# Kernel tuning notes

Hardware: AMD Instinct MI355X
Metric: run time of the kernel (lower is better)

## Reference

```python
import jax, jax.numpy as jnp
import numpy as np

V, S, B, D, H, DH, FF = 98304, 1536, 2, 768, 24, 32, 3072
SCALE = 1.0 / float(np.sqrt(DH))  # 0.17677669529663687


def _ln(x, w, b, eps=1e-5):
    mu = jnp.mean(x, axis=-1, keepdims=True)
    var = jnp.mean(jnp.square(x - mu), axis=-1, keepdims=True)
    return (x - mu) * jax.lax.rsqrt(var + eps) * w + b


def _block(x, mask, ln1w, ln1b, wqkv, bqkv, wo, bo, ln2w, ln2b, wfc, bfc, wproj, bproj):
    # x: (S, B, D) Megatron layout; mask: (B, 1, S, S) bool, True = masked
    h = _ln(x, ln1w, ln1b)
    qkv = (h @ wqkv.T + bqkv).reshape(S, B, H, 3 * DH)  # interleaved q/k/v per head
    q, k, v = qkv[..., :DH], qkv[..., DH:2 * DH], qkv[..., 2 * DH:]
    q = jnp.transpose(q, (1, 2, 0, 3))  # (B, H, S, DH)
    k = jnp.transpose(k, (1, 2, 0, 3))
    v = jnp.transpose(v, (1, 2, 0, 3))
    scores = jnp.einsum('bhqd,bhkd->bhqk', q, k) * SCALE  # (B, H, S, S)
    scores = jnp.where(mask, jnp.float32(-10000.0), scores)
    p = jax.nn.softmax(scores, axis=-1)
    ctx = jnp.einsum('bhqk,bhkd->bhqd', p, v)
    ctx = jnp.transpose(ctx, (2, 0, 1, 3)).reshape(S, B, D)  # back to (S, B, D)
    x = x + ctx @ wo.T + bo  # attention residual (dropout treated as identity)
    h2 = _ln(x, ln2w, ln2b)
    m = jax.nn.gelu(h2 @ wfc.T + bfc, approximate=False)  # exact (erf) gelu as aten.gelu
    return x + m @ wproj.T + bproj


def _param_shapes():
    ps = [('wte', (V, D)), ('wpe', (S, D))]
    for l in ('l0', 'l1'):
        ps += [(l + '_ln1_w', (D,)), (l + '_ln1_b', (D,)),
               (l + '_wqkv', (3 * D, D)), (l + '_bqkv', (3 * D,)),
               (l + '_wo', (D, D)), (l + '_bo', (D,)),
               (l + '_ln2_w', (D,)), (l + '_ln2_b', (D,)),
               (l + '_wfc', (FF, D)), (l + '_bfc', (FF,)),
               (l + '_wproj', (D, FF)), (l + '_bproj', (D,))]
    ps += [('lnf_w', (D,)), ('lnf_b', (D,))]
    return ps


def setup_inputs() -> dict:
    key = jax.random.key(0)
    inp = {}
    inp['input_ids'] = jax.random.randint(jax.random.fold_in(key, 0), (B, S), 0, V, dtype=jnp.int32)
    inp['position_ids'] = jnp.broadcast_to(jnp.arange(S, dtype=jnp.int32), (B, S))
    causal = jnp.triu(jnp.ones((S, S), jnp.bool_), k=1)  # True above diagonal = masked
    inp['attn_mask'] = jnp.broadcast_to(causal, (B, 1, S, S))
    for i, (name, shape) in enumerate(_param_shapes()):
        k = jax.random.fold_in(key, 100 + i)
        if name in ('lnf_w',) or (('_ln' in name) and name.endswith('_w')):
            inp[name] = jnp.ones(shape, jnp.float32)
        else:
            inp[name] = jax.random.normal(k, shape, jnp.float32) * 0.02
    return inp


def reference(input_ids, position_ids, attn_mask,
              wte, wpe,
              l0_ln1_w, l0_ln1_b, l0_wqkv, l0_bqkv, l0_wo, l0_bo,
              l0_ln2_w, l0_ln2_b, l0_wfc, l0_bfc, l0_wproj, l0_bproj,
              l1_ln1_w, l1_ln1_b, l1_wqkv, l1_bqkv, l1_wo, l1_bo,
              l1_ln2_w, l1_ln2_b, l1_wfc, l1_bfc, l1_wproj, l1_bproj,
              lnf_w, lnf_b):
    x = wte[input_ids] + wpe[position_ids]  # (B, S, D)
    x = jnp.transpose(x, (1, 0, 2))  # (S, B, D)
    x = _block(x, attn_mask, l0_ln1_w, l0_ln1_b, l0_wqkv, l0_bqkv, l0_wo, l0_bo,
               l0_ln2_w, l0_ln2_b, l0_wfc, l0_bfc, l0_wproj, l0_bproj)
    x = _block(x, attn_mask, l1_ln1_w, l1_ln1_b, l1_wqkv, l1_bqkv, l1_wo, l1_bo,
               l1_ln2_w, l1_ln2_b, l1_wfc, l1_bfc, l1_wproj, l1_bproj)
    return _ln(x, lnf_w, lnf_b)  # (S, B, D)
```

## Files before the change

kernel.cpp:

```cpp
#include <hip/hip_runtime.h>
#include <cmath>
#include <type_traits>

typedef unsigned short u16;
typedef float  f32x4 __attribute__((ext_vector_type(4)));
typedef short  s16x8 __attribute__((ext_vector_type(8)));
typedef __bf16 b16x8 __attribute__((ext_vector_type(8)));

constexpr int S_  = 1536;
constexpr int B_  = 2;
constexpr int D_  = 768;
constexpr int H_  = 24;
constexpr int DH_ = 32;
constexpr int FF_ = 3072;
constexpr int N_  = S_ * B_;
constexpr int D3_ = 3 * D_;
constexpr float SCALE_ = 0.17677669529663687f;

template <typename T>
static __device__ inline auto mfma_try(T a, T b, f32x4 c, int)
    -> decltype(__builtin_amdgcn_mfma_f32_16x16x32_bf16(a, b, c, 0, 0, 0)) {
  return __builtin_amdgcn_mfma_f32_16x16x32_bf16(a, b, c, 0, 0, 0);
}
template <typename T>
static __device__ inline f32x4 mfma_try(T a, T b, f32x4 c, long) {
  b16x8 ab = __builtin_bit_cast(b16x8, a);
  b16x8 bb = __builtin_bit_cast(b16x8, b);
  return __builtin_amdgcn_mfma_f32_16x16x32_bf16(ab, bb, c, 0, 0, 0);
}
static __device__ inline f32x4 mfma_bf16(s16x8 a, s16x8 b, f32x4 c) {
  return mfma_try(a, b, c, 0);
}

static __device__ inline u16 f2bf(float f) {
  unsigned u = __builtin_bit_cast(unsigned, f);
  return (u16)((u + 0x7FFFu + ((u >> 16) & 1u)) >> 16);
}

static __device__ inline float rmax16(float v) {
  v = fmaxf(v, __shfl_xor(v, 1));
  v = fmaxf(v, __shfl_xor(v, 2));
  v = fmaxf(v, __shfl_xor(v, 4));
  v = fmaxf(v, __shfl_xor(v, 8));
  return v;
}
static __device__ inline float rsum16(float v) {
  v += __shfl_xor(v, 1);
  v += __shfl_xor(v, 2);
  v += __shfl_xor(v, 4);
  v += __shfl_xor(v, 8);
  return v;
}

__global__ void convert_weights_kernel(const float* __restrict__ wqkv,
                                       const float* __restrict__ wo,
                                       const float* __restrict__ wfc,
                                       const float* __restrict__ wproj,
                                       u16* __restrict__ dst) {
  constexpr int C0 = D3_ * D_;
  constexpr int C1 = C0 + D_ * D_;
  constexpr int C2 = C1 + FF_ * D_;
  constexpr int C3 = C2 + D_ * FF_;
  int i4 = (blockIdx.x * 256 + threadIdx.x) * 4;
  if (i4 >= C3) return;
  const float* src; int off;
  if (i4 < C0)      { src = wqkv;  off = i4; }
  else if (i4 < C1) { src = wo;    off = i4 - C0; }
  else if (i4 < C2) { src = wfc;   off = i4 - C1; }
  else              { src = wproj; off = i4 - C2; }
  float4 v = *(const float4*)(src + off);
  ushort4 o;
  o.x = f2bf(v.x); o.y = f2bf(v.y); o.z = f2bf(v.z); o.w = f2bf(v.w);
  *(ushort4*)(dst + i4) = o;
}

__global__ void embed_kernel(const int* __restrict__ ids, const int* __restrict__ pos,
                             const float* __restrict__ wte, const float* __restrict__ wpe,
                             float* __restrict__ x) {
  int g  = blockIdx.x * 256 + threadIdx.x;
  int i4 = g * 4;
  int row = i4 / D_;
  int d   = i4 - row * D_;
  int s = row >> 1, b = row & 1;
  int t = ids[b * S_ + s];
  int p = pos[b * S_ + s];
  float4 a = *(const float4*)(wte + (size_t)t * D_ + d);
  float4 c = *(const float4*)(wpe + (size_t)p * D_ + d);
  a.x += c.x; a.y += c.y; a.z += c.z; a.w += c.w;
  *(float4*)(x + i4) = a;
}

template <typename OUT>
__global__ void ln_kernel(const float* __restrict__ x, const float* __restrict__ w,
                          const float* __restrict__ b, OUT* __restrict__ out) {
  int wid = threadIdx.x >> 6, lane = threadIdx.x & 63;
  int tok = blockIdx.x * 4 + wid;
  const float* xr = x + (size_t)tok * D_;
  float4 v[3];
  float s = 0.f, ss = 0.f;
#pragma unroll
  for (int c = 0; c < 3; ++c) {
    v[c] = *(const float4*)(xr + c * 256 + lane * 4);
    s  += v[c].x + v[c].y + v[c].z + v[c].w;
    ss += v[c].x * v[c].x + v[c].y * v[c].y + v[c].z * v[c].z + v[c].w * v[c].w;
  }
#pragma unroll
  for (int m = 1; m <= 32; m <<= 1) { s += __shfl_xor(s, m); ss += __shfl_xor(ss, m); }
  float mu = s * (1.0f / D_);
  float var = ss * (1.0f / D_) - mu * mu;
  float rs = rsqrtf(var + 1e-5f);
#pragma unroll
  for (int c = 0; c < 3; ++c) {
    int d = c * 256 + lane * 4;
    float o0 = (v[c].x - mu) * rs * w[d + 0] + b[d + 0];
    float o1 = (v[c].y - mu) * rs * w[d + 1] + b[d + 1];
    float o2 = (v[c].z - mu) * rs * w[d + 2] + b[d + 2];
    float o3 = (v[c].w - mu) * rs * w[d + 3] + b[d + 3];
    if constexpr (std::is_same_v<OUT, u16>) {
      ushort4 o; o.x = f2bf(o0); o.y = f2bf(o1); o.z = f2bf(o2); o.w = f2bf(o3);
      *(ushort4*)(out + (size_t)tok * D_ + d) = o;
    } else {
      float4 o; o.x = o0; o.y = o1; o.z = o2; o.w = o3;
      *(float4*)(out + (size_t)tok * D_ + d) = o;
    }
  }
}

template <int BM, int BN, int EPI>
__launch_bounds__(256, 2)
__global__ void gemm_kernel(const u16* __restrict__ X, const u16* __restrict__ W,
                            const float* __restrict__ bias, int K,
                            u16* __restrict__ o0, u16* __restrict__ o1,
                            u16* __restrict__ o2, float* __restrict__ xio) {
  constexpr int AS = 40;
  constexpr int WM = BM / 2, WN = BN / 2, TM = WM / 16, TN = WN / 16;
  __shared__ u16 As[BM * AS];
  __shared__ u16 Bs[BN * AS];
  const int tid = threadIdx.x;
  const int wid = tid >> 6, lane = tid & 63;
  const int col = lane & 15, quad = lane >> 4;
  const int wm = wid & 1, wn = wid >> 1;
  const int rowA0 = blockIdx.x * BM;
  const int rowB0 = blockIdx.y * BN;

  f32x4 zz = {0.f, 0.f, 0.f, 0.f};
  f32x4 acc[TM][TN];
#pragma unroll
  for (int i = 0; i < TM; ++i)
#pragma unroll
    for (int j = 0; j < TN; ++j) acc[i][j] = zz;

  for (int k0 = 0; k0 < K; k0 += 32) {
#pragma unroll
    for (int it = 0; it < BM / 64; ++it) {
      int slot = tid + it * 256;
      int r = slot >> 2, c = slot & 3;
      *(uint4*)&As[r * AS + c * 8] = *(const uint4*)&X[(size_t)(rowA0 + r) * K + k0 + c * 8];
    }
#pragma unroll
    for (int it = 0; it < BN / 64; ++it) {
      int slot = tid + it * 256;
      int r = slot >> 2, c = slot & 3;
      *(uint4*)&Bs[r * AS + c * 8] = *(const uint4*)&W[(size_t)(rowB0 + r) * K + k0 + c * 8];
    }
    __syncthreads();
    s16x8 af[TM], bf[TN];
#pragma unroll
    for (int ti = 0; ti < TM; ++ti)
      af[ti] = *(const s16x8*)&As[(wm * WM + ti * 16 + col) * AS + quad * 8];
#pragma unroll
    for (int tj = 0; tj < TN; ++tj)
      bf[tj] = *(const s16x8*)&Bs[(wn * WN + tj * 16 + col) * AS + quad * 8];
#pragma unroll
    for (int ti = 0; ti < TM; ++ti)
#pragma unroll
      for (int tj = 0; tj < TN; ++tj)
        acc[ti][tj] = mfma_bf16(af[ti], bf[tj], acc[ti][tj]);
    __syncthreads();
  }

  const int tokBase  = rowA0 + wm * WM + quad * 4;
  const int featBase = rowB0 + wn * WN + col;
#pragma unroll
  for (int ti = 0; ti < TM; ++ti) {
#pragma unroll
    for (int tj = 0; tj < TN; ++tj) {
      int feat = featBase + tj * 16;
      float bv = bias[feat];
#pragma unroll
      for (int r = 0; r < 4; ++r) {
        int tok = tokBase + ti * 16 + r;
        float v = acc[ti][tj][r] + bv;
        if constexpr (EPI == 0) {
          int hh = feat / 96;
          int rem = feat - hh * 96;
          int comp = rem >> 5, d = rem & 31;
          int s = tok >> 1, bb = tok & 1;
          int bh = bb * H_ + hh;
          if (comp == 0)      o0[((size_t)bh * S_ + s) * DH_ + d] = f2bf(v);
          else if (comp == 1) o1[((size_t)bh * S_ + s) * DH_ + d] = f2bf(v);
          else                o2[((size_t)bh * DH_ + d) * S_ + s] = f2bf(v);
        } else if constexpr (EPI == 1) {
          float* p = xio + (size_t)tok * D_ + feat;
          *p = *p + v;
        } else {
          float g = 0.5f * v * (1.0f + erff(v * 0.70710678118654752f));
          o0[(size_t)tok * FF_ + feat] = f2bf(g);
        }
      }
    }
  }
}

__launch_bounds__(256)
__global__ void attn_kernel(const u16* __restrict__ q, const u16* __restrict__ k,
                            const u16* __restrict__ vt, u16* __restrict__ ctx) {
  __shared__ u16 Plds[4][16 * 40];
  const int tid = threadIdx.x;
  const int wid = tid >> 6, lane = tid & 63;
  const int col = lane & 15, quad = lane >> 4;
  const int bh = blockIdx.y;
  const int bb = bh / H_, hh = bh - bb * H_;
  const u16* qb = q  + (size_t)bh * S_ * DH_;
  const u16* kb = k  + (size_t)bh * S_ * DH_;
  const u16* vb = vt + (size_t)bh * DH_ * S_;
  const int q0 = blockIdx.x * 64 + wid * 16;

  s16x8 qf = *(const s16x8*)&qb[(q0 + col) * DH_ + quad * 8];
  f32x4 zz = {0.f, 0.f, 0.f, 0.f};
  f32x4 o0 = zz, o1 = zz;
  float mr[4] = {-1e30f, -1e30f, -1e30f, -1e30f};
  float lr[4] = {0.f, 0.f, 0.f, 0.f};

  const int kend = blockIdx.x * 64 + 64;
  for (int k0 = 0; k0 < kend; k0 += 32) {
    s16x8 kf0 = *(const s16x8*)&kb[(k0 + col) * DH_ + quad * 8];
    s16x8 kf1 = *(const s16x8*)&kb[(k0 + 16 + col) * DH_ + quad * 8];
    f32x4 s0 = mfma_bf16(qf, kf0, zz);
    f32x4 s1 = mfma_bf16(qf, kf1, zz);
#pragma unroll
    for (int r = 0; r < 4; ++r) {
      int qq = q0 + quad * 4 + r;
      float x0 = (k0 + col <= qq)      ? s0[r] * SCALE_ : -10000.0f;
      float x1 = (k0 + 16 + col <= qq) ? s1[r] * SCALE_ : -10000.0f;
      float cm = rmax16(fmaxf(x0, x1));
      float nm = fmaxf(mr[r], cm);
      float al = __expf(mr[r] - nm);
      float p0 = __expf(x0 - nm);
      float p1 = __expf(x1 - nm);
      float rs = rsum16(p0 + p1);
      lr[r] = lr[r] * al + rs;
      mr[r] = nm;
      o0[r] *= al; o1[r] *= al;
      Plds[wid][(quad * 4 + r) * 40 + col]      = f2bf(p0);
      Plds[wid][(quad * 4 + r) * 40 + 16 + col] = f2bf(p1);
    }
    __syncthreads();
    s16x8 pf  = *(const s16x8*)&Plds[wid][col * 40 + quad * 8];
    s16x8 vf0 = *(const s16x8*)&vb[(size_t)col * S_ + k0 + quad * 8];
    s16x8 vf1 = *(const s16x8*)&vb[(size_t)(16 + col) * S_ + k0 + quad * 8];
    o0 = mfma_bf16(pf, vf0, o0);
    o1 = mfma_bf16(pf, vf1, o1);
    __syncthreads();
  }
#pragma unroll
  for (int r = 0; r < 4; ++r) {
    int qq = q0 + quad * 4 + r;
    float inv = 1.0f / lr[r];
    size_t base = ((size_t)qq * B_ + bb) * D_ + hh * DH_;
    ctx[base + col]      = f2bf(o0[r] * inv);
    ctx[base + 16 + col] = f2bf(o1[r] * inv);
  }
}

extern "C" void kernel_launch(void* const* d_in, const int* in_sizes, int n_in,
                              void* d_out, int out_size, void* d_ws, size_t ws_size,
                              hipStream_t stream) {
  const int*   ids = (const int*)d_in[0];
  const int*   pos = (const int*)d_in[1];
  const float* wte = (const float*)d_in[3];
  const float* wpe = (const float*)d_in[4];
  const float* lnf_w = (const float*)d_in[29];
  const float* lnf_b = (const float*)d_in[30];

  char* ws = (char*)d_ws;
  constexpr size_t SZ_X   = (size_t)N_ * D_ * 4;
  constexpr size_t SZ_H   = (size_t)N_ * D_ * 2;
  constexpr size_t SZ_QKV = (size_t)B_ * H_ * S_ * DH_ * 2;
  constexpr size_t SZ_M   = (size_t)N_ * FF_ * 2;
  constexpr int    WELEM  = D3_ * D_ + D_ * D_ + FF_ * D_ + D_ * FF_;

  float* xbuf = (float*)ws;
  u16* hbuf  = (u16*)(ws + SZ_X);
  u16* qbuf  = (u16*)(ws + SZ_X + SZ_H);
  u16* kbuf  = (u16*)(ws + SZ_X + SZ_H + SZ_QKV);
  u16* vtbuf = (u16*)(ws + SZ_X + SZ_H + 2 * SZ_QKV);
  u16* cbuf  = (u16*)(ws + SZ_X + SZ_H + 3 * SZ_QKV);
  u16* mbuf  = (u16*)(ws + SZ_X + SZ_H + 4 * SZ_QKV);
  u16* wbf   = (u16*)(ws + SZ_X + SZ_H + 4 * SZ_QKV + SZ_M);

  embed_kernel<<<N_ * D_ / 4 / 256, 256, 0, stream>>>(ids, pos, wte, wpe, xbuf);

  for (int l = 0; l < 2; ++l) {
    int p = 5 + l * 12;
    const float* ln1w  = (const float*)d_in[p + 0];
    const float* ln1b  = (const float*)d_in[p + 1];
    const float* wqkv  = (const float*)d_in[p + 2];
    const float* bqkv  = (const float*)d_in[p + 3];
    const float* wo    = (const float*)d_in[p + 4];
    const float* bo    = (const float*)d_in[p + 5];
    const float* ln2w  = (const float*)d_in[p + 6];
    const float* ln2b  = (const float*)d_in[p + 7];
    const float* wfc   = (const float*)d_in[p + 8];
    const float* bfc   = (const float*)d_in[p + 9];
    const float* wproj = (const float*)d_in[p + 10];
    const float* bproj = (const float*)d_in[p + 11];

    u16* wb = wbf + (size_t)l * WELEM;
    u16* wqkv_b  = wb;
    u16* wo_b    = wb + D3_ * D_;
    u16* wfc_b   = wb + D3_ * D_ + D_ * D_;
    u16* wproj_b = wb + D3_ * D_ + D_ * D_ + FF_ * D_;

    convert_weights_kernel<<<WELEM / 4 / 256, 256, 0, stream>>>(wqkv, wo, wfc, wproj, wb);

    ln_kernel<u16><<<N_ / 4, 256, 0, stream>>>(xbuf, ln1w, ln1b, hbuf);
    gemm_kernel<128, 128, 0><<<dim3(N_ / 128, D3_ / 128), 256, 0, stream>>>(
        hbuf, wqkv_b, bqkv, D_, qbuf, kbuf, vtbuf, nullptr);
    attn_kernel<<<dim3(S_ / 64, B_ * H_), 256, 0, stream>>>(qbuf, kbuf, vtbuf, cbuf);
    gemm_kernel<128, 64, 1><<<dim3(N_ / 128, D_ / 64), 256, 0, stream>>>(
        cbuf, wo_b, bo, D_, nullptr, nullptr, nullptr, xbuf);
    ln_kernel<u16><<<N_ / 4, 256, 0, stream>>>(xbuf, ln2w, ln2b, hbuf);
    gemm_kernel<128, 128, 2><<<dim3(N_ / 128, FF_ / 128), 256, 0, stream>>>(
        hbuf, wfc_b, bfc, D_, mbuf, nullptr, nullptr, nullptr);
    gemm_kernel<128, 64, 1><<<dim3(N_ / 128, D_ / 64), 256, 0, stream>>>(
        mbuf, wproj_b, bproj, FF_, nullptr, nullptr, nullptr, xbuf);
  }

  ln_kernel<float><<<N_ / 4, 256, 0, stream>>>(xbuf, lnf_w, lnf_b, (float*)d_out);
}
```

Before: 943.9 us.

## Use direct global-to-LDS loads with swizzle in GEMM, trim attention causal loop and barriers

The GEMM now loads tiles with global_load_lds (direct global-to-LDS DMA) into an XOR-swizzled LDS layout with BK=64, and raises the launch-bounds occupancy hint from 2 to 3. The swizzle avoids bank conflicts without padding, and the larger K step halves the number of barrier pairs per tile. In attention, each wave stops at its own causal limit instead of the block's, and the block-wide __syncthreads are replaced by wave-local barriers plus an LDS waitcnt, since each wave only touches its own P slice. The risks are register pressure from the occupancy hint and correctness of the hand-written waitcnt encoding.

```diff
diff --git a/kernel.cpp b/kernel.cpp
--- a/kernel.cpp
+++ b/kernel.cpp
@@ -6,6 +6,9 @@
 typedef float  f32x4 __attribute__((ext_vector_type(4)));
 typedef short  s16x8 __attribute__((ext_vector_type(8)));
 typedef __bf16 b16x8 __attribute__((ext_vector_type(8)));
+
+#define GLOBAL_AS __attribute__((address_space(1)))
+#define LDS_AS    __attribute__((address_space(3)))
 
 constexpr int S_  = 1536;
 constexpr int B_  = 2;
@@ -127,15 +130,15 @@
 }
 
 template <int BM, int BN, int EPI>
-__launch_bounds__(256, 2)
+__launch_bounds__(256, 3)
 __global__ void gemm_kernel(const u16* __restrict__ X, const u16* __restrict__ W,
                             const float* __restrict__ bias, int K,
                             u16* __restrict__ o0, u16* __restrict__ o1,
                             u16* __restrict__ o2, float* __restrict__ xio) {
-  constexpr int AS = 40;
+  constexpr int BK = 64;
   constexpr int WM = BM / 2, WN = BN / 2, TM = WM / 16, TN = WN / 16;
-  __shared__ u16 As[BM * AS];
-  __shared__ u16 Bs[BN * AS];
+  __shared__ u16 As[BM * BK];
+  __shared__ u16 Bs[BN * BK];
   const int tid = threadIdx.x;
   const int wid = tid >> 6, lane = tid & 63;
   const int col = lane & 15, quad = lane >> 4;
@@ -150,32 +153,47 @@
 #pragma unroll
     for (int j = 0; j < TN; ++j) acc[i][j] = zz;
 
-  for (int k0 = 0; k0 < K; k0 += 32) {
-#pragma unroll
-    for (int it = 0; it < BM / 64; ++it) {
-      int slot = tid + it * 256;
-      int r = slot >> 2, c = slot & 3;
-      *(uint4*)&As[r * AS + c * 8] = *(const uint4*)&X[(size_t)(rowA0 + r) * K + k0 + c * 8];
-    }
-#pragma unroll
-    for (int it = 0; it < BN / 64; ++it) {
-      int slot = tid + it * 256;
-      int r = slot >> 2, c = slot & 3;
-      *(uint4*)&Bs[r * AS + c * 8] = *(const uint4*)&W[(size_t)(rowB0 + r) * K + k0 + c * 8];
+  for (int k0 = 0; k0 < K; k0 += BK) {
+#pragma unroll
+    for (int it = 0; it < BM / 32; ++it) {
+      int bs = (it * 4 + wid) * 64;
+      int slot = bs + lane;
+      int r = slot >> 3;
+      int c = (slot & 7) ^ (r & 7);
+      const u16* g = &X[(size_t)(rowA0 + r) * K + k0 + c * 8];
+      __builtin_amdgcn_global_load_lds((const GLOBAL_AS unsigned int*)g,
+                                       (LDS_AS unsigned int*)&As[bs * 8], 16, 0, 0);
+    }
+#pragma unroll
+    for (int it = 0; it < BN / 32; ++it) {
+      int bs = (it * 4 + wid) * 64;
+      int slot = bs + lane;
+      int r = slot >> 3;
+      int c = (slot & 7) ^ (r & 7);
+      const u16* g = &W[(size_t)(rowB0 + r) * K + k0 + c * 8];
+      __builtin_amdgcn_global_load_lds((const GLOBAL_AS unsigned int*)g,
+                                       (LDS_AS unsigned int*)&Bs[bs * 8], 16, 0, 0);
     }
     __syncthreads();
-    s16x8 af[TM], bf[TN];
-#pragma unroll
-    for (int ti = 0; ti < TM; ++ti)
-      af[ti] = *(const s16x8*)&As[(wm * WM + ti * 16 + col) * AS + quad * 8];
-#pragma unroll
-    for (int tj = 0; tj < TN; ++tj)
-      bf[tj] = *(const s16x8*)&Bs[(wn * WN + tj * 16 + col) * AS + quad * 8];
-#pragma unroll
-    for (int ti = 0; ti < TM; ++ti)
-#pragma unroll
-      for (int tj = 0; tj < TN; ++tj)
-        acc[ti][tj] = mfma_bf16(af[ti], bf[tj], acc[ti][tj]);
+#pragma unroll
+    for (int kb = 0; kb < 2; ++kb) {
+      s16x8 af[TM], bf[TN];
+#pragma unroll
+      for (int ti = 0; ti < TM; ++ti) {
+        int row = wm * WM + ti * 16 + col;
+        af[ti] = *(const s16x8*)&As[row * BK + ((kb * 4 + quad) ^ (row & 7)) * 8];
+      }
+#pragma unroll
+      for (int tj = 0; tj < TN; ++tj) {
+        int row = wn * WN + tj * 16 + col;
+        bf[tj] = *(const s16x8*)&Bs[row * BK + ((kb * 4 + quad) ^ (row & 7)) * 8];
+      }
+#pragma unroll
+      for (int ti = 0; ti < TM; ++ti)
+#pragma unroll
+        for (int tj = 0; tj < TN; ++tj)
+          acc[ti][tj] = mfma_bf16(af[ti], bf[tj], acc[ti][tj]);
+    }
     __syncthreads();
   }
 
@@ -232,7 +250,7 @@
   float mr[4] = {-1e30f, -1e30f, -1e30f, -1e30f};
   float lr[4] = {0.f, 0.f, 0.f, 0.f};
 
-  const int kend = blockIdx.x * 64 + 64;
+  const int kend = q0 + 16;
   for (int k0 = 0; k0 < kend; k0 += 32) {
     s16x8 kf0 = *(const s16x8*)&kb[(k0 + col) * DH_ + quad * 8];
     s16x8 kf1 = *(const s16x8*)&kb[(k0 + 16 + col) * DH_ + quad * 8];
@@ -255,18 +273,20 @@
       Plds[wid][(quad * 4 + r) * 40 + col]      = f2bf(p0);
       Plds[wid][(quad * 4 + r) * 40 + 16 + col] = f2bf(p1);
     }
-    __syncthreads();
+    __builtin_amdgcn_wave_barrier();
+    __builtin_amdgcn_s_waitcnt(0xc07f);
+    __builtin_amdgcn_wave_barrier();
     s16x8 pf  = *(const s16x8*)&Plds[wid][col * 40 + quad * 8];
     s16x8 vf0 = *(const s16x8*)&vb[(size_t)col * S_ + k0 + quad * 8];
     s16x8 vf1 = *(const s16x8*)&vb[(size_t)(16 + col) * S_ + k0 + quad * 8];
     o0 = mfma_bf16(pf, vf0, o0);
     o1 = mfma_bf16(pf, vf1, o1);
-    __syncthreads();
+    __builtin_amdgcn_wave_barrier();
   }
 #pragma unroll
   for (int r = 0; r < 4; ++r) {
+    float inv = 1.0f / lr[r];
     int qq = q0 + quad * 4 + r;
-    float inv = 1.0f / lr[r];
     size_t base = ((size_t)qq * B_ + bb) * D_ + hh * DH_;
     ctx[base + col]      = f2bf(o0[r] * inv);
     ctx[base + 16 + col] = f2bf(o1[r] * inv);
```

New measurement: 840.0 us. 1.12x faster.
